# Kernel optimization log

Hardware: AMD Instinct MI355X
Metric: run time of the kernel (lower is better)

Reference implementation:

```python
import jax, jax.numpy as jnp
import numpy as np

EPS = 1e-6


def _feature_map(x):
    # elu(x) + 1
    return jax.nn.elu(x) + 1.0


def _causal_dot(Qb, Kb, V):
    """Causal linear attention numerator for 3 stacked branches.
    Qb, Kb: [3, N, L, H, D]; V: [N, L, H, Dv] -> out [3, N, L, H, Dv].
    out[b,n,l,h,:] = sum_{s<=l} (Qb[b,n,l,h,:] . Kb[b,n,s,h,:]) V[n,s,h,:]
    computed with an O(L) recurrent scan over cumulative KV outer products.
    """
    Qs = jnp.moveaxis(Qb, 2, 0)  # [L, 3, N, H, D]
    Ks = jnp.moveaxis(Kb, 2, 0)  # [L, 3, N, H, D]
    Vs = jnp.moveaxis(V, 1, 0)   # [L, N, H, Dv]
    B, N, _, H, D = Qb.shape
    Dv = V.shape[-1]
    S0 = jnp.zeros((B, N, H, D, Dv), dtype=Qb.dtype)

    def step(S, inp):
        q, k, v = inp  # q,k: [3,N,H,D], v: [N,H,Dv]
        S = S + k[..., :, None] * v[None, :, :, None, :]
        o = jnp.einsum('bnhi,bnhij->bnhj', q, S)
        return S, o

    _, out = jax.lax.scan(step, S0, (Qs, Ks, Vs))  # out: [L,3,N,H,Dv]
    return jnp.moveaxis(out, 0, 2)  # [3,N,L,H,Dv]


def setup_inputs() -> dict:
    key = jax.random.key(0)
    ks = jax.random.split(key, 5)
    N, L, H, D = 4, 2048, 8, 128
    return {
        'queries': jax.random.normal(ks[0], (N, L, H, D), dtype=jnp.float32),
        'q2': jax.random.normal(ks[1], (N, L, H, D), dtype=jnp.float32),
        'keys': jax.random.normal(ks[2], (N, L, H, D), dtype=jnp.float32),
        'values': jax.random.normal(ks[3], (N, L, H, D), dtype=jnp.float32),
        'key_lengths': jnp.ones((N, L), dtype=jnp.float32),
        'omega': jax.random.normal(ks[4], (H, D, D), dtype=jnp.float32),
    }


def reference(queries, q2, keys, values, key_lengths, omega):
    N, L, H, D = queries.shape
    Q = _feature_map(queries)                       # [N,L,H,D]
    K = _feature_map(keys) * key_lengths[:, :, None, None]

    # Delta[n,l,h,i] = l/L for all n,h,i -> projection through omega reduces to
    # (l/L) * sum_i omega[h,i,j], same math as einsum('nlhi,hij->nlhj', Delta, omega).
    delta = (jnp.arange(L, dtype=queries.dtype) / L)        # [L]
    t = delta[:, None, None] * jnp.sum(omega, axis=1)[None]  # [L,H,D]
    sin_t, cos_t = jnp.sin(t), jnp.cos(t)
    s2, c2, sc = sin_t ** 2, cos_t ** 2, sin_t * cos_t       # [L,H,D] each

    # Q_term = sin(phi(q2))^2 * feature_map(queries)
    q2_proj = jnp.einsum('nlhi,hij->nlhj', q2, omega)
    Q_term = (jnp.sin(q2_proj) ** 2) * Q                     # [N,L,H,D]

    # Branch trig weights: Q gets [sin^2, cos^2, sin*cos], K gets [cos^2, sin^2, sin*cos]
    wq = jnp.stack([s2, c2, sc])[:, None]  # [3,1,L,H,D]
    wk = jnp.stack([c2, s2, sc])[:, None]
    Qb = Q_term[None] * wq                 # [3,N,L,H,D]
    Kb = K[None] * wk                      # [3,N,L,H,D]

    # Denominator terms Z_b = <Q_b[l], cumsum_{s<=l} K_b[s]>
    Kcum = jnp.cumsum(Kb, axis=2)
    Z = jnp.einsum('bnlhi,bnlhi->bnlh', Qb, Kcum)   # [3,N,L,H]

    Vb = _causal_dot(Qb, Kb, values)                # [3,N,L,H,D]

    numerator = Vb[0] + Vb[1] - 2.0 * Vb[2]
    denominator = Z[0] + Z[1] - 2.0 * Z[2] + EPS
    return numerator / denominator[:, :, :, None]
```

## Files before the change

kernel.cpp:

```cpp
#include <hip/hip_runtime.h>


typedef float f32x4 __attribute__((ext_vector_type(4)));
typedef short s16x8 __attribute__((ext_vector_type(8)));
typedef short s16x4 __attribute__((ext_vector_type(4)));
typedef unsigned short u16;

static constexpr int    Ln   = 2048;
static constexpr size_t NHLD = (size_t)32 * 2048 * 128;
static constexpr size_t KSB  = (size_t)32 * 16 * 128;

__device__ __forceinline__ float b2f(u16 s) {
  union { unsigned u; float f; } x; x.u = ((unsigned)s) << 16; return x.f;
}
__device__ __forceinline__ u16 f2b(float f) {
  union { float f; unsigned u; } x; x.f = f;
  unsigned r = x.u + 0x7fffu + ((x.u >> 16) & 1u);
  return (u16)(r >> 16);
}
__device__ __forceinline__ s16x8 pack8(f32x4 a, f32x4 b) {
  s16x8 r;
  r[0] = (short)f2b(a[0]); r[1] = (short)f2b(a[1]); r[2] = (short)f2b(a[2]); r[3] = (short)f2b(a[3]);
  r[4] = (short)f2b(b[0]); r[5] = (short)f2b(b[1]); r[6] = (short)f2b(b[2]); r[7] = (short)f2b(b[3]);
  return r;
}

__global__ __launch_bounds__(256) void k_omega(const float* __restrict__ om,
                                               u16* __restrict__ wt, float* __restrict__ osum) {
  __shared__ alignas(16) u16 T[128][136];
  int h = blockIdx.x, t = threadIdx.x;
  for (int idx = t; idx < 128 * 32; idx += 256) {
    int i = idx >> 5, cs = (idx & 31) << 2;
    f32x4 vv = *(const f32x4*)(om + ((size_t)(h * 128 + i)) * 128 + cs);
    T[i][cs + 0] = f2b(vv[0]); T[i][cs + 1] = f2b(vv[1]);
    T[i][cs + 2] = f2b(vv[2]); T[i][cs + 3] = f2b(vv[3]);
  }
  if (t < 128) {
    float acc = 0.f;
    for (int i = 0; i < 128; i++) acc += om[((size_t)(h * 128 + i)) * 128 + t];
    osum[h * 128 + t] = acc;
  }
  __syncthreads();
  {
    int j = t >> 1, lh = (t & 1) << 6;
    s16x8* dst = (s16x8*)(wt + ((size_t)(h * 128 + j)) * 128 + lh);
    for (int u = 0; u < 8; u++) {
      s16x8 pv;
#pragma unroll
      for (int e = 0; e < 8; e++) pv[e] = (short)T[lh + u * 8 + e][j];
      dst[u] = pv;
    }
  }
}

__global__ __launch_bounds__(512) void k_kvs(const float* __restrict__ kg, const float* __restrict__ vg,
                                             const float* __restrict__ klg, const float* __restrict__ osum,
                                             u16* __restrict__ kb3, u16* __restrict__ vt,
                                             u16* __restrict__ sct, float* __restrict__ ksum) {
  __shared__ union {
    alignas(16) u16 VT[128][128];
    alignas(16) u16 KT[128][136];
  } sm;
  int bid = blockIdx.x, t = threadIdx.x;
  int c = bid & 15, h = (bid >> 4) & 7, n = bid >> 7;
  int l0 = c << 7, nh = (n << 3) + h;
  const float invL = 1.0f / 2048.0f;
  int gcol = t & 31, cs = gcol << 2;
  f32x4 osv = *(const f32x4*)(osum + h * 128 + cs);
#pragma unroll
  for (int it = 0; it < 8; it++) {
    int rr = (it << 4) + (t >> 5);
    int l = l0 + rr;
    size_t gb = (((size_t)(n * Ln + l) * 8 + h) << 7) + cs;
    f32x4 kv = *(const f32x4*)(kg + gb);
    f32x4 vv = *(const f32x4*)(vg + gb);
    float klv = klg[n * Ln + l];
    float tb = (float)l * invL;
    u16 r0[4], r1[4], r2[4];
#pragma unroll
    for (int e = 0; e < 4; e++) {
      float kf = (kv[e] > 0.f ? kv[e] + 1.f : __expf(kv[e])) * klv;
      float tt = tb * osv[e];
      float s, cc; __sincosf(tt, &s, &cc);
      r0[e] = f2b(kf * cc * cc);
      r1[e] = f2b(kf * s * s);
      r2[e] = f2b(kf * s * cc);
    }
    int gs = (gcol ^ (rr >> 3)) << 2;
    *(s16x4*)&sm.VT[rr][gs] = (s16x4){(short)f2b(vv[0]), (short)f2b(vv[1]),
                                      (short)f2b(vv[2]), (short)f2b(vv[3])};
    size_t nb = ((size_t)nh * Ln + l) * 128 + cs;
    *(s16x4*)(kb3 + nb)          = (s16x4){(short)r0[0], (short)r0[1], (short)r0[2], (short)r0[3]};
    *(s16x4*)(kb3 + NHLD + nb)   = (s16x4){(short)r1[0], (short)r1[1], (short)r1[2], (short)r1[3]};
    *(s16x4*)(kb3 + 2*NHLD + nb) = (s16x4){(short)r2[0], (short)r2[1], (short)r2[2], (short)r2[3]};
  }
  __syncthreads();
  size_t bv = ((size_t)(nh * 16 + c)) << 14;
  for (int idx = t; idx < 2048; idx += 512) {
    int i = idx >> 4, o = idx & 15;
    int gp = (((i >> 2) ^ o) << 2) + (i & 3);
    s16x8 v1;
#pragma unroll
    for (int u = 0; u < 8; u++) v1[u] = (short)sm.VT[(o << 3) + u][gp];
    *(s16x8*)(vt + bv + (((size_t)i) << 7) + (o << 3)) = v1;
  }
  int lane = t & 63, quad = lane >> 4, nl = lane & 15, w = t >> 6;
  int arow = (w << 4) + nl;
  const u16* vchunk = vt + bv;
  for (int b = 0; b < 3; b++) {
    int bnh = b * 32 + nh;
    const u16* kb = kb3 + (size_t)b * NHLD + ((size_t)nh * Ln + l0) * 128;
    __syncthreads();
    for (int idx = t; idx < 2048; idx += 512) {
      int s = idx >> 4, io = idx & 15;
      s16x8 v = *(const s16x8*)(kb + (((size_t)s) << 7) + (io << 3));
      int cp = s ^ ((io & 7) << 3);
#pragma unroll
      for (int j = 0; j < 8; j++) sm.KT[(io << 3) + j][cp] = (u16)(short)v[j];
    }
    __syncthreads();
    f32x4 z4 = {0.f, 0.f, 0.f, 0.f};
    f32x4 acc[8];
#pragma unroll
    for (int i = 0; i < 8; i++) acc[i] = z4;
    for (int ks = 0; ks < 4; ks++) {
      int k0 = (ks << 5) + (quad << 3);
      s16x8 av = *(const s16x8*)(vchunk + (((size_t)arow) << 7) + k0);
#pragma unroll
      for (int ct = 0; ct < 8; ct++) {
        int r = (ct << 4) + nl;
        int koff = k0 ^ (((r >> 3) & 7) << 3);
        s16x8 bvv = *(const s16x8*)&sm.KT[r][koff];
        acc[ct] = __builtin_amdgcn_mfma_f32_16x16x32_bf16(av, bvv, acc[ct], 0, 0, 0);
      }
    }
    if (t < 128) {
      float s = 0.f;
      int sw = ((t >> 3) & 7) << 3;
#pragma unroll 4
      for (int g = 0; g < 128; g += 8) {
        s16x8 v = *(const s16x8*)&sm.KT[t][g ^ sw];
#pragma unroll
        for (int e = 0; e < 8; e++) s += b2f((u16)v[e]);
      }
      ksum[(size_t)(bnh * 16 + c) * 128 + t] = s;
    }
    __syncthreads();
    {
      int lbase = (w << 4) + (quad << 2);
#pragma unroll
      for (int ct = 0; ct < 8; ct++) {
        int i = (ct << 4) + nl;
#pragma unroll
        for (int r = 0; r < 4; r++) sm.KT[lbase + r][i] = f2b(acc[ct][r]);
      }
    }
    __syncthreads();
    size_t sbase = ((size_t)(bnh * 16 + c)) << 14;
    for (int idx = t; idx < 2048; idx += 512) {
      int jr = idx >> 4, g = (idx & 15) << 3;
      *(s16x8*)(sct + sbase + ((size_t)jr << 7) + g) = *(const s16x8*)&sm.KT[jr][g];
    }
  }
}

__global__ __launch_bounds__(256) void p1b(u16* __restrict__ sct, float* __restrict__ ksum) {
  int bid = blockIdx.x, t = threadIdx.x;
  if (bid < 768) {
    int tid = bid * 256 + t;
    int bnh = tid >> 11, rem = tid & 2047;
    size_t base = ((size_t)bnh << 18) + ((size_t)rem << 3);
    float acc[8] = {0.f, 0.f, 0.f, 0.f, 0.f, 0.f, 0.f, 0.f};
    for (int c = 0; c < 16; c++) {
      size_t a = base + ((size_t)c << 14);
      s16x8 v = *(const s16x8*)(sct + a);
      s16x8 o;
#pragma unroll
      for (int e = 0; e < 8; e++) { o[e] = (short)f2b(acc[e]); acc[e] += b2f((u16)v[e]); }
      *(s16x8*)(sct + a) = o;
    }
  } else {
    int m2 = (bid - 768) * 256 + t;
    int i = m2 & 127, bnh = m2 >> 7;
    size_t base = (size_t)bnh * 2048 + i;
    float acc = 0.f;
    for (int c = 0; c < 16; c++) {
      size_t a = base + (size_t)c * 128;
      float v = ksum[a];
      ksum[a] = acc;
      acc += v;
    }
  }
}

__global__ __launch_bounds__(256, 2) void k_qfeat(const float* __restrict__ q2g, const float* __restrict__ qg,
                                                  const u16* __restrict__ wt, const float* __restrict__ osum,
                                                  const float* __restrict__ kspre,
                                                  u16* __restrict__ qb3, float* __restrict__ zintg) {
  __shared__ alignas(16) u16 B[128][136];
  __shared__ float osb[128];
  int bid = blockIdx.x, t = threadIdx.x;
  int m = bid & 31, h = (bid >> 5) & 7, n = bid >> 8;
  int l0 = m << 6, c = m >> 1, nh = (n << 3) + h;
  if (t < 128) osb[t] = osum[h * 128 + t];
  for (int idx = t; idx < 2048; idx += 256) {
    int j = idx >> 4, cs = (idx & 15) << 3;
    *(s16x8*)&B[j][cs] = *(const s16x8*)(wt + ((size_t)(h * 128 + j)) * 128 + cs);
  }
  __syncthreads();
  int lane = t & 63, quad = lane >> 4, nl = lane & 15, w = t >> 6;
  f32x4 z4 = {0.f, 0.f, 0.f, 0.f};
  f32x4 acc[8];
#pragma unroll
  for (int i = 0; i < 8; i++) acc[i] = z4;
  int arow = l0 + (w << 4) + nl;
  for (int ks = 0; ks < 4; ks++) {
    int k0 = (ks << 5) + (quad << 3);
    const float* ap = q2g + (((size_t)(n * Ln + arow) * 8 + h) << 7) + k0;
    s16x8 av = pack8(*(const f32x4*)ap, *(const f32x4*)(ap + 4));
#pragma unroll
    for (int ct = 0; ct < 8; ct++) {
      s16x8 bv = *(const s16x8*)&B[(ct << 4) + nl][k0];
      acc[ct] = __builtin_amdgcn_mfma_f32_16x16x32_bf16(av, bv, acc[ct], 0, 0, 0);
    }
  }
  __syncthreads();
  {
    int lbase = (w << 4) + (quad << 2);
#pragma unroll
    for (int ct = 0; ct < 8; ct++) {
      int j = (ct << 4) + nl;
#pragma unroll
      for (int r = 0; r < 4; r++) {
        float sp = __sinf(acc[ct][r]);
        B[lbase + r][j] = f2b(sp * sp);
      }
    }
  }
  __syncthreads();
  const float invL = 1.0f / 2048.0f;
  for (int idx = t; idx < 1024; idx += 256) {
    int l = idx >> 4, j0 = (idx & 15) << 3, gl = l0 + l;
    s16x8 s2v = *(const s16x8*)&B[l][j0];
    const float* qp = qg + (((size_t)(n * Ln + gl) * 8 + h) << 7) + j0;
    f32x4 qa = *(const f32x4*)qp, qbv = *(const f32x4*)(qp + 4);
    size_t kbb = ((size_t)nh * 16 + c) * 128 + j0;
    f32x4 kp0a = *(const f32x4*)(kspre + kbb),           kp0b = *(const f32x4*)(kspre + kbb + 4);
    f32x4 kp1a = *(const f32x4*)(kspre + kbb + KSB),     kp1b = *(const f32x4*)(kspre + kbb + KSB + 4);
    f32x4 kp2a = *(const f32x4*)(kspre + kbb + 2 * KSB), kp2b = *(const f32x4*)(kspre + kbb + 2 * KSB + 4);
    s16x8 o0, o1, o2;
    float z = 0.f;
    float tb = (float)gl * invL;
#pragma unroll
    for (int e = 0; e < 8; e++) {
      float s2p = b2f((u16)s2v[e]);
      float qv = (e < 4) ? qa[e] : qbv[e - 4];
      float f = qv > 0.f ? qv + 1.f : __expf(qv);
      float Qt = s2p * f;
      float tt = tb * osb[j0 + e];
      float s, cc; __sincosf(tt, &s, &cc);
      float v0 = Qt * s * s, v1 = Qt * cc * cc, v2 = -2.f * Qt * s * cc;
      float k0v = (e < 4) ? kp0a[e] : kp0b[e - 4];
      float k1v = (e < 4) ? kp1a[e] : kp1b[e - 4];
      float k2v = (e < 4) ? kp2a[e] : kp2b[e - 4];
      z += v0 * k0v + v1 * k1v + v2 * k2v;
      o0[e] = (short)f2b(v0); o1[e] = (short)f2b(v1); o2[e] = (short)f2b(v2);
    }
    size_t base = ((size_t)nh * Ln + gl) * 128 + j0;
    *(s16x8*)(qb3 + base)            = o0;
    *(s16x8*)(qb3 + base + NHLD)     = o1;
    *(s16x8*)(qb3 + base + 2 * NHLD) = o2;
    z += __shfl_xor(z, 1); z += __shfl_xor(z, 2);
    z += __shfl_xor(z, 4); z += __shfl_xor(z, 8);
    if (nl == 0) zintg[(size_t)nh * Ln + gl] = z;
  }
}

__global__ __launch_bounds__(512, 4) void p3(const u16* __restrict__ qb3, const u16* __restrict__ kb3,
                                             const u16* __restrict__ vtg, const u16* __restrict__ sct,
                                             const float* __restrict__ zintg, float* __restrict__ outg) {
  __shared__ union {
    struct { alignas(16) u16 T0[128][128]; alignas(16) u16 T1[128][128]; } s;
    alignas(16) float O[128][132];
  } sm;
  int bid = blockIdx.x, t = threadIdx.x;
  int c = bid & 15, h = (bid >> 4) & 7, n = bid >> 7;
  int l0c = c << 7, nh = (n << 3) + h;
  int lane = t & 63, quad = lane >> 4, nl = lane & 15, w = t >> 6;
  f32x4 z4 = {0.f, 0.f, 0.f, 0.f};
  f32x4 accP[8], accO[8];
#pragma unroll
  for (int i = 0; i < 8; i++) { accP[i] = z4; accO[i] = z4; }
  int arow = l0c + (w << 4) + nl;
  for (int b = 0; b < 3; b++) {
    int bnh = b * 32 + nh;
    __syncthreads();
    for (int idx = t; idx < 2048; idx += 512) {
      int s = idx >> 4;
      int co = (((idx & 15) ^ (s & 7)) << 3);
      *(s16x8*)&sm.s.T0[s][co] = *(const s16x8*)(kb3 + (((size_t)bnh * Ln + l0c + s) << 7) + ((idx & 15) << 3));
    }
    size_t sbase = ((size_t)(bnh * 16 + c)) << 14;
    for (int idx = t; idx < 2048; idx += 512) {
      int j = idx >> 4;
      int co = (((idx & 15) ^ (j & 7)) << 3);
      *(s16x8*)&sm.s.T1[j][co] = *(const s16x8*)(sct + sbase + ((size_t)j << 7) + ((idx & 15) << 3));
    }
    s16x8 av[4];
#pragma unroll
    for (int ks = 0; ks < 4; ks++)
      av[ks] = *(const s16x8*)(qb3 + (((size_t)bnh * Ln + arow) << 7) + (ks << 5) + (quad << 3));
    __syncthreads();
    for (int ks = 0; ks < 4; ks++) {
      int k0 = (ks << 5) + (quad << 3);
#pragma unroll
      for (int ct = 0; ct < 8; ct++) {
        int r = (ct << 4) + nl;
        int koff = k0 ^ ((r & 7) << 3);
        s16x8 bv0 = *(const s16x8*)&sm.s.T0[r][koff];
        accP[ct] = __builtin_amdgcn_mfma_f32_16x16x32_bf16(av[ks], bv0, accP[ct], 0, 0, 0);
        s16x8 bv1 = *(const s16x8*)&sm.s.T1[r][koff];
        accO[ct] = __builtin_amdgcn_mfma_f32_16x16x32_bf16(av[ks], bv1, accO[ct], 0, 0, 0);
      }
    }
  }
  __syncthreads();
  float zP[4] = {0.f, 0.f, 0.f, 0.f};
  int lbase = (w << 4) + (quad << 2);
#pragma unroll
  for (int ct = 0; ct < 8; ct++) {
    int ss = (ct << 4) + nl;
#pragma unroll
    for (int r = 0; r < 4; r++) {
      int lr = lbase + r;
      float pv = (ss <= lr) ? accP[ct][r] : 0.f;
      zP[r] += pv;
      sm.s.T0[lr][ss ^ ((lr & 7) << 3)] = f2b(pv);
    }
  }
#pragma unroll
  for (int mteam = 1; mteam <= 8; mteam <<= 1) {
#pragma unroll
    for (int r = 0; r < 4; r++) zP[r] += __shfl_xor(zP[r], mteam);
  }
  size_t vbase = ((size_t)(nh * 16 + c)) << 14;
  for (int idx = t; idx < 2048; idx += 512) {
    int j = idx >> 4;
    int co = (((idx & 15) ^ (j & 7)) << 3);
    *(s16x8*)&sm.s.T1[j][co] = *(const s16x8*)(vtg + vbase + ((size_t)idx << 3));
  }
  float zf[4];
#pragma unroll
  for (int r = 0; r < 4; r++)
    zf[r] = zintg[(size_t)nh * Ln + l0c + lbase + r] + zP[r] + 1e-6f;
  __syncthreads();
  for (int ks = 0; ks < 4; ks++) {
    int k0 = (ks << 5) + (quad << 3);
    int rw = (w << 4) + nl;
    s16x8 pav = *(const s16x8*)&sm.s.T0[rw][k0 ^ ((rw & 7) << 3)];
#pragma unroll
    for (int ct = 0; ct < 8; ct++) {
      int r = (ct << 4) + nl;
      s16x8 vv = *(const s16x8*)&sm.s.T1[r][k0 ^ ((r & 7) << 3)];
      accO[ct] = __builtin_amdgcn_mfma_f32_16x16x32_bf16(pav, vv, accO[ct], 0, 0, 0);
    }
  }
  __syncthreads();
#pragma unroll
  for (int ct = 0; ct < 8; ct++) {
    int j = (ct << 4) + nl;
#pragma unroll
    for (int r = 0; r < 4; r++) sm.O[lbase + r][j] = accO[ct][r] / zf[r];
  }
  __syncthreads();
  for (int idx = t; idx < 4096; idx += 512) {
    int l = idx >> 5, g = (idx & 31) << 2;
    *(f32x4*)(outg + (((size_t)(n * Ln + l0c + l) * 8 + h) << 7) + g) = *(const f32x4*)&sm.O[l][g];
  }
}

extern "C" void kernel_launch(void* const* d_in, const int* in_sizes, int n_in,
                              void* d_out, int out_size, void* d_ws, size_t ws_size,
                              hipStream_t stream) {
  (void)in_sizes; (void)n_in; (void)out_size; (void)ws_size;
  const float* q   = (const float*)d_in[0];
  const float* q2  = (const float*)d_in[1];
  const float* kk  = (const float*)d_in[2];
  const float* vv  = (const float*)d_in[3];
  const float* kl  = (const float*)d_in[4];
  const float* om  = (const float*)d_in[5];
  float* out = (float*)d_out;

  u16* W     = (u16*)d_ws;
  u16* qb3   = W;
  u16* kb3   = W + 3 * NHLD;
  u16* vt    = W + 6 * NHLD;
  u16* sct   = W + 7 * NHLD;
  u16* wt    = W + 10 * NHLD;
  float* ks  = (float*)(W + 10 * NHLD + 131072);
  float* osm = ks + 196608;
  float* zin = osm + 1024;

  k_omega <<<8,    256, 0, stream>>>(om, wt, osm);
  k_kvs   <<<512,  512, 0, stream>>>(kk, vv, kl, osm, kb3, vt, sct, ks);
  p1b     <<<816,  256, 0, stream>>>(sct, ks);
  k_qfeat <<<1024, 256, 0, stream>>>(q2, q, wt, osm, ks, qb3, zin);
  p3      <<<512,  512, 0, stream>>>(qb3, kb3, vt, sct, zin, out);
}
```

Measured before the change: 269.2 us.

## Fuse query feature kernel into final attention kernel, dropping qb3 round-trip

```diff
diff --git a/kernel.cpp b/kernel.cpp
--- a/kernel.cpp
+++ b/kernel.cpp
@@ -193,62 +193,71 @@
   }
 }
 
-__global__ __launch_bounds__(256, 2) void k_qfeat(const float* __restrict__ q2g, const float* __restrict__ qg,
-                                                  const u16* __restrict__ wt, const float* __restrict__ osum,
-                                                  const float* __restrict__ kspre,
-                                                  u16* __restrict__ qb3, float* __restrict__ zintg) {
-  __shared__ alignas(16) u16 B[128][136];
+__global__ __launch_bounds__(512, 4) void p3(const float* __restrict__ q2g, const float* __restrict__ qg,
+                                             const u16* __restrict__ wtg, const float* __restrict__ osum,
+                                             const float* __restrict__ kspre,
+                                             const u16* __restrict__ kb3, const u16* __restrict__ vtg,
+                                             const u16* __restrict__ sct, float* __restrict__ outg) {
+  __shared__ union {
+    struct { alignas(16) u16 T0[128][128]; alignas(16) u16 T1[128][128]; } s;
+    alignas(16) float O[128][132];
+  } sm;
+  __shared__ float zl[128];
   __shared__ float osb[128];
   int bid = blockIdx.x, t = threadIdx.x;
-  int m = bid & 31, h = (bid >> 5) & 7, n = bid >> 8;
-  int l0 = m << 6, c = m >> 1, nh = (n << 3) + h;
+  int c = bid & 15, h = (bid >> 4) & 7, n = bid >> 7;
+  int l0c = c << 7, nh = (n << 3) + h;
+  int lane = t & 63, quad = lane >> 4, nl = lane & 15, w = t >> 6;
+  const float invL = 1.0f / 2048.0f;
   if (t < 128) osb[t] = osum[h * 128 + t];
-  for (int idx = t; idx < 2048; idx += 256) {
-    int j = idx >> 4, cs = (idx & 15) << 3;
-    *(s16x8*)&B[j][cs] = *(const s16x8*)(wt + ((size_t)(h * 128 + j)) * 128 + cs);
-  }
-  __syncthreads();
-  int lane = t & 63, quad = lane >> 4, nl = lane & 15, w = t >> 6;
+  for (int idx = t; idx < 2048; idx += 512) {
+    int j = idx >> 4;
+    int co = (((idx & 15) ^ (j & 7)) << 3);
+    *(s16x8*)&sm.s.T1[j][co] = *(const s16x8*)(wtg + ((size_t)(h * 128 + j)) * 128 + ((idx & 15) << 3));
+  }
+  __syncthreads();
   f32x4 z4 = {0.f, 0.f, 0.f, 0.f};
-  f32x4 acc[8];
-#pragma unroll
-  for (int i = 0; i < 8; i++) acc[i] = z4;
-  int arow = l0 + (w << 4) + nl;
+  f32x4 accP[8], accO[8];
+#pragma unroll
+  for (int i = 0; i < 8; i++) { accP[i] = z4; accO[i] = z4; }
+  int arow = l0c + (w << 4) + nl;
   for (int ks = 0; ks < 4; ks++) {
     int k0 = (ks << 5) + (quad << 3);
     const float* ap = q2g + (((size_t)(n * Ln + arow) * 8 + h) << 7) + k0;
-    s16x8 av = pack8(*(const f32x4*)ap, *(const f32x4*)(ap + 4));
+    s16x8 avq = pack8(*(const f32x4*)ap, *(const f32x4*)(ap + 4));
 #pragma unroll
     for (int ct = 0; ct < 8; ct++) {
-      s16x8 bv = *(const s16x8*)&B[(ct << 4) + nl][k0];
-      acc[ct] = __builtin_amdgcn_mfma_f32_16x16x32_bf16(av, bv, acc[ct], 0, 0, 0);
-    }
-  }
-  __syncthreads();
-  {
-    int lbase = (w << 4) + (quad << 2);
-#pragma unroll
-    for (int ct = 0; ct < 8; ct++) {
-      int j = (ct << 4) + nl;
-#pragma unroll
-      for (int r = 0; r < 4; r++) {
-        float sp = __sinf(acc[ct][r]);
-        B[lbase + r][j] = f2b(sp * sp);
-      }
-    }
-  }
-  __syncthreads();
-  const float invL = 1.0f / 2048.0f;
-  for (int idx = t; idx < 1024; idx += 256) {
-    int l = idx >> 4, j0 = (idx & 15) << 3, gl = l0 + l;
-    s16x8 s2v = *(const s16x8*)&B[l][j0];
+      int r = (ct << 4) + nl;
+      s16x8 bv = *(const s16x8*)&sm.s.T1[r][k0 ^ ((r & 7) << 3)];
+      accP[ct] = __builtin_amdgcn_mfma_f32_16x16x32_bf16(avq, bv, accP[ct], 0, 0, 0);
+    }
+  }
+  __syncthreads();
+  int lbase = (w << 4) + (quad << 2);
+#pragma unroll
+  for (int ct = 0; ct < 8; ct++) {
+    int j = (ct << 4) + nl;
+#pragma unroll
+    for (int r = 0; r < 4; r++) {
+      int row = lbase + r;
+      float sp = __sinf(accP[ct][r]);
+      sm.s.T0[row][((((j >> 3) ^ (row & 7)) << 3) | (j & 7))] = f2b(sp * sp);
+    }
+  }
+  __syncthreads();
+  s16x8 s2r[4];
+#pragma unroll
+  for (int it = 0; it < 4; it++) {
+    int idx = t + (it << 9);
+    int l = idx >> 4, oct = idx & 15, j0 = oct << 3, gl = l0c + l;
+    s16x8 s2v = *(const s16x8*)&sm.s.T0[l][(oct ^ (l & 7)) << 3];
+    s2r[it] = s2v;
     const float* qp = qg + (((size_t)(n * Ln + gl) * 8 + h) << 7) + j0;
     f32x4 qa = *(const f32x4*)qp, qbv = *(const f32x4*)(qp + 4);
     size_t kbb = ((size_t)nh * 16 + c) * 128 + j0;
     f32x4 kp0a = *(const f32x4*)(kspre + kbb),           kp0b = *(const f32x4*)(kspre + kbb + 4);
     f32x4 kp1a = *(const f32x4*)(kspre + kbb + KSB),     kp1b = *(const f32x4*)(kspre + kbb + KSB + 4);
     f32x4 kp2a = *(const f32x4*)(kspre + kbb + 2 * KSB), kp2b = *(const f32x4*)(kspre + kbb + 2 * KSB + 4);
-    s16x8 o0, o1, o2;
     float z = 0.f;
     float tb = (float)gl * invL;
 #pragma unroll
@@ -264,52 +273,63 @@
       float k1v = (e < 4) ? kp1a[e] : kp1b[e - 4];
       float k2v = (e < 4) ? kp2a[e] : kp2b[e - 4];
       z += v0 * k0v + v1 * k1v + v2 * k2v;
-      o0[e] = (short)f2b(v0); o1[e] = (short)f2b(v1); o2[e] = (short)f2b(v2);
-    }
-    size_t base = ((size_t)nh * Ln + gl) * 128 + j0;
-    *(s16x8*)(qb3 + base)            = o0;
-    *(s16x8*)(qb3 + base + NHLD)     = o1;
-    *(s16x8*)(qb3 + base + 2 * NHLD) = o2;
+    }
     z += __shfl_xor(z, 1); z += __shfl_xor(z, 2);
     z += __shfl_xor(z, 4); z += __shfl_xor(z, 8);
-    if (nl == 0) zintg[(size_t)nh * Ln + gl] = z;
-  }
-}
-
-__global__ __launch_bounds__(512, 4) void p3(const u16* __restrict__ qb3, const u16* __restrict__ kb3,
-                                             const u16* __restrict__ vtg, const u16* __restrict__ sct,
-                                             const float* __restrict__ zintg, float* __restrict__ outg) {
-  __shared__ union {
-    struct { alignas(16) u16 T0[128][128]; alignas(16) u16 T1[128][128]; } s;
-    alignas(16) float O[128][132];
-  } sm;
-  int bid = blockIdx.x, t = threadIdx.x;
-  int c = bid & 15, h = (bid >> 4) & 7, n = bid >> 7;
-  int l0c = c << 7, nh = (n << 3) + h;
-  int lane = t & 63, quad = lane >> 4, nl = lane & 15, w = t >> 6;
-  f32x4 z4 = {0.f, 0.f, 0.f, 0.f};
-  f32x4 accP[8], accO[8];
-#pragma unroll
-  for (int i = 0; i < 8; i++) { accP[i] = z4; accO[i] = z4; }
-  int arow = l0c + (w << 4) + nl;
+    if (nl == 0) zl[l] = z;
+  }
+#pragma unroll
+  for (int i = 0; i < 8; i++) accP[i] = z4;
   for (int b = 0; b < 3; b++) {
     int bnh = b * 32 + nh;
     __syncthreads();
+#pragma unroll
+    for (int it = 0; it < 4; it++) {
+      int idx = t + (it << 9);
+      int l = idx >> 4, oct = idx & 15, j0 = oct << 3, gl = l0c + l;
+      s16x8 s2v = s2r[it];
+      const float* qp = qg + (((size_t)(n * Ln + gl) * 8 + h) << 7) + j0;
+      f32x4 qa = *(const f32x4*)qp, qbv = *(const f32x4*)(qp + 4);
+      float tb = (float)gl * invL;
+      s16x8 o;
+#pragma unroll
+      for (int e = 0; e < 8; e++) {
+        float s2p = b2f((u16)s2v[e]);
+        float qv = (e < 4) ? qa[e] : qbv[e - 4];
+        float f = qv > 0.f ? qv + 1.f : __expf(qv);
+        float Qt = s2p * f;
+        float tt = tb * osb[j0 + e];
+        float s, cc; __sincosf(tt, &s, &cc);
+        float vb;
+        if (b == 0) vb = Qt * s * s;
+        else if (b == 1) vb = Qt * cc * cc;
+        else vb = -2.f * Qt * s * cc;
+        o[e] = (short)f2b(vb);
+      }
+      *(s16x8*)&sm.s.T1[l][(oct ^ (l & 7)) << 3] = o;
+    }
+    __syncthreads();
+    s16x8 av[4];
+    {
+      int rl = (w << 4) + nl;
+#pragma unroll
+      for (int ks = 0; ks < 4; ks++) {
+        int k0 = (ks << 5) + (quad << 3);
+        av[ks] = *(const s16x8*)&sm.s.T1[rl][k0 ^ ((rl & 7) << 3)];
+      }
+    }
     for (int idx = t; idx < 2048; idx += 512) {
       int s = idx >> 4;
       int co = (((idx & 15) ^ (s & 7)) << 3);
       *(s16x8*)&sm.s.T0[s][co] = *(const s16x8*)(kb3 + (((size_t)bnh * Ln + l0c + s) << 7) + ((idx & 15) << 3));
     }
+    __syncthreads();
     size_t sbase = ((size_t)(bnh * 16 + c)) << 14;
     for (int idx = t; idx < 2048; idx += 512) {
       int j = idx >> 4;
       int co = (((idx & 15) ^ (j & 7)) << 3);
       *(s16x8*)&sm.s.T1[j][co] = *(const s16x8*)(sct + sbase + ((size_t)j << 7) + ((idx & 15) << 3));
     }
-    s16x8 av[4];
-#pragma unroll
-    for (int ks = 0; ks < 4; ks++)
-      av[ks] = *(const s16x8*)(qb3 + (((size_t)bnh * Ln + arow) << 7) + (ks << 5) + (quad << 3));
     __syncthreads();
     for (int ks = 0; ks < 4; ks++) {
       int k0 = (ks << 5) + (quad << 3);
@@ -326,7 +346,6 @@
   }
   __syncthreads();
   float zP[4] = {0.f, 0.f, 0.f, 0.f};
-  int lbase = (w << 4) + (quad << 2);
 #pragma unroll
   for (int ct = 0; ct < 8; ct++) {
     int ss = (ct << 4) + nl;
@@ -352,7 +371,7 @@
   float zf[4];
 #pragma unroll
   for (int r = 0; r < 4; r++)
-    zf[r] = zintg[(size_t)nh * Ln + l0c + lbase + r] + zP[r] + 1e-6f;
+    zf[r] = zl[lbase + r] + zP[r] + 1e-6f;
   __syncthreads();
   for (int ks = 0; ks < 4; ks++) {
     int k0 = (ks << 5) + (quad << 3);
@@ -392,18 +411,15 @@
   float* out = (float*)d_out;
 
   u16* W     = (u16*)d_ws;
-  u16* qb3   = W;
-  u16* kb3   = W + 3 * NHLD;
-  u16* vt    = W + 6 * NHLD;
-  u16* sct   = W + 7 * NHLD;
-  u16* wt    = W + 10 * NHLD;
-  float* ks  = (float*)(W + 10 * NHLD + 131072);
+  u16* kb3   = W;
+  u16* vt    = W + 3 * NHLD;
+  u16* sct   = W + 4 * NHLD;
+  u16* wt    = W + 7 * NHLD;
+  float* ks  = (float*)(W + 7 * NHLD + 131072);
   float* osm = ks + 196608;
-  float* zin = osm + 1024;
 
   k_omega <<<8,    256, 0, stream>>>(om, wt, osm);
   k_kvs   <<<512,  512, 0, stream>>>(kk, vv, kl, osm, kb3, vt, sct, ks);
   p1b     <<<816,  256, 0, stream>>>(sct, ks);
-  k_qfeat <<<1024, 256, 0, stream>>>(q2, q, wt, osm, ks, qb3, zin);
-  p3      <<<512,  512, 0, stream>>>(qb3, kb3, vt, sct, zin, out);
-}
+  p3      <<<512,  512, 0, stream>>>(q2, q, wt, osm, ks, kb3, vt, sct, out);
+}
```

Result: slower. 293.5 us (+9.0%).
